# Kernel tuning notes

Measured on AMD Instinct MI355X. Metric: run time of the kernel, lower is better.

The kernel has to match this reference:

```python
import jax, jax.numpy as jnp
import numpy as np

B, L, D_IN, D_OUT = 4, 2048, 4096, 4096


def setup_inputs() -> dict:
    key = jax.random.key(0)
    k1, k2, k3, k4 = jax.random.split(key, 4)
    x = jax.random.normal(k1, (B, L, D_IN), dtype=jnp.float32)
    # base weight stored transposed as [in, out], like self.base = base.T
    base = jax.random.normal(k2, (D_IN, D_OUT), dtype=jnp.float32) * 0.02
    # binary delta sign mask in {0, 1}, stored transposed [in, out]
    mask = jax.random.randint(k3, (D_IN, D_OUT), 0, 2).astype(jnp.int32)
    # coeff = mean(|finetune - base|); a small positive scalar
    coeff = jax.random.uniform(k4, (1,), dtype=jnp.float32) * 0.01
    return {"x": x, "base": base, "coeff": coeff, "mask": mask}


def reference(x, base, coeff, mask):
    # Original: x @ base.T_stored + coeff * (x @ repeated_mask)
    # (t_coeff * x) @ mask == t_coeff * (x @ mask); we avoid materializing the
    # per-batch repeated mask since broadcasting the [in, out] mask is equivalent.
    m = mask.astype(x.dtype)            # {0,1} dequantized mask, [in, out]
    c = coeff[0].astype(x.dtype)
    return jnp.einsum('bld,de->ble', x, base) + c * jnp.einsum('bld,de->ble', x, m)
```

## Files before the change

kernel.cpp:

```cpp
#include <hip/hip_runtime.h>
#include <hip/hip_bf16.h>
#include <stdint.h>

#define DIN 4096
#define DOUT 4096
#define BK 64
#define NT (DIN / BK)

typedef __attribute__((ext_vector_type(8))) short short8;
typedef __attribute__((ext_vector_type(8))) unsigned short ushort8;
typedef __attribute__((ext_vector_type(4))) float f32x4;

__device__ inline unsigned short f2bf(float f) {
    union { float f; unsigned u; } v; v.f = f;
    unsigned r = v.u + 0x7fffu + ((v.u >> 16) & 1u);
    return (unsigned short)(r >> 16);
}

__global__ void cvt_x_kernel(const float* __restrict__ x, ushort* __restrict__ xb, long n8) {
    long i = (long)blockIdx.x * blockDim.x + threadIdx.x;
    if (i >= n8) return;
    const float4* p = (const float4*)(x + i * 8);
    float4 v0 = p[0], v1 = p[1];
    ushort8 o;
    o[0] = f2bf(v0.x); o[1] = f2bf(v0.y); o[2] = f2bf(v0.z); o[3] = f2bf(v0.w);
    o[4] = f2bf(v1.x); o[5] = f2bf(v1.y); o[6] = f2bf(v1.z); o[7] = f2bf(v1.w);
    *(ushort8*)(xb + i * 8) = o;
}

__global__ void make_wt_kernel(const float* __restrict__ base, const int* __restrict__ mask,
                               const float* __restrict__ coeff, ushort* __restrict__ wt) {
    __shared__ float tile[64][65];
    const float c = coeff[0];
    const int t = threadIdx.x;
    const int bd = blockIdx.x >> 6;
    const int be = blockIdx.x & 63;
    const int d0 = bd * 64, e0 = be * 64;
#pragma unroll
    for (int i = 0; i < 4; ++i) {
        int idx = i * 256 + t;
        int r = idx >> 4;
        int c4 = (idx & 15) << 2;
        const float4 bv = *(const float4*)(base + (size_t)(d0 + r) * DOUT + e0 + c4);
        const int4  mv = *(const int4*)(mask + (size_t)(d0 + r) * DOUT + e0 + c4);
        tile[r][c4 + 0] = bv.x + c * (float)mv.x;
        tile[r][c4 + 1] = bv.y + c * (float)mv.y;
        tile[r][c4 + 2] = bv.z + c * (float)mv.z;
        tile[r][c4 + 3] = bv.w + c * (float)mv.w;
    }
    __syncthreads();
#pragma unroll
    for (int i = 0; i < 8; ++i) {
        int idx = i * 256 + t;
        int r = idx >> 5;
        int p = (idx & 31) << 1;
        ushort2 o;
        o.x = f2bf(tile[p][r]);
        o.y = f2bf(tile[p + 1][r]);
        *(ushort2*)(wt + (size_t)(e0 + r) * DIN + d0 + p) = o;
    }
}


#define MFMA(d, va, vb) d = __builtin_amdgcn_mfma_f32_16x16x32_bf16(va, vb, d, 0, 0, 0)

#define GLL(P, L) \
    __builtin_amdgcn_global_load_lds( \
        (const __attribute__((address_space(1))) void*)(P), \
        (__attribute__((address_space(3))) void*)(L), 16, 0, 0)

#define RDA(BUF,KK,OH,MM) (*(const short8*)&lA[BUF][KK][aoff + (OH)*2048 + (MM)*512])
#define RDB(BUF,KK,NN)    (*(const short8*)&lB[BUF][KK][boff + (NN)*512])

#define STAGE_A(BUF,KK,OFE) { GLL(gA0 + (OFE), &lA[BUF][KK][doff]); \
                              GLL(gA1 + (OFE), &lA[BUF][KK][doff + 4096]); }
#define STAGE_B(BUF,KK,OFE) { GLL(gB0 + (OFE), &lB[BUF][KK][doff]); \
                              GLL(gB1 + (OFE), &lB[BUF][KK][doff + 4096]); }

#define PHASE_CORE(AOFF) \
    __builtin_amdgcn_s_barrier(); \
    asm volatile("s_waitcnt lgkmcnt(0)" ::: "memory"); \
    __builtin_amdgcn_sched_barrier(0); \
    __builtin_amdgcn_s_setprio(1); \
    MFMA(acc[AOFF+0][0],a0,b0); MFMA(acc[AOFF+0][1],a0,b1); MFMA(acc[AOFF+0][2],a0,b2); MFMA(acc[AOFF+0][3],a0,b3); \
    MFMA(acc[AOFF+1][0],a1,b0); MFMA(acc[AOFF+1][1],a1,b1); MFMA(acc[AOFF+1][2],a1,b2); MFMA(acc[AOFF+1][3],a1,b3); \
    MFMA(acc[AOFF+2][0],a2,b0); MFMA(acc[AOFF+2][1],a2,b1); MFMA(acc[AOFF+2][2],a2,b2); MFMA(acc[AOFF+2][3],a2,b3); \
    MFMA(acc[AOFF+3][0],a3,b0); MFMA(acc[AOFF+3][1],a3,b1); MFMA(acc[AOFF+3][2],a3,b2); MFMA(acc[AOFF+3][3],a3,b3); \
    __builtin_amdgcn_s_setprio(0);

#define KTILE(BUF, G1, G2, NEXT, OFE1, OFE2) \
  { \
    short8 a0,a1,a2,a3,b0,b1,b2,b3; \
    a0=RDA(BUF,0,0,0); a1=RDA(BUF,0,0,1); a2=RDA(BUF,0,0,2); a3=RDA(BUF,0,0,3); \
    b0=RDB(BUF,0,0); b1=RDB(BUF,0,1); b2=RDB(BUF,0,2); b3=RDB(BUF,0,3); \
    if (G1) STAGE_A(1-(BUF), 1, OFE1) \
    PHASE_CORE(0) \
    __builtin_amdgcn_s_barrier(); \
    a0=RDA(BUF,0,1,0); a1=RDA(BUF,0,1,1); a2=RDA(BUF,0,1,2); a3=RDA(BUF,0,1,3); \
    if (G1) STAGE_B(1-(BUF), 1, OFE1) \
    PHASE_CORE(4) \
    __builtin_amdgcn_s_barrier(); \
    a0=RDA(BUF,1,0,0); a1=RDA(BUF,1,0,1); a2=RDA(BUF,1,0,2); a3=RDA(BUF,1,0,3); \
    b0=RDB(BUF,1,0); b1=RDB(BUF,1,1); b2=RDB(BUF,1,2); b3=RDB(BUF,1,3); \
    if (G2) STAGE_A(BUF, 0, OFE2) \
    PHASE_CORE(0) \
    __builtin_amdgcn_s_barrier(); \
    a0=RDA(BUF,1,1,0); a1=RDA(BUF,1,1,1); a2=RDA(BUF,1,1,2); a3=RDA(BUF,1,1,3); \
    if (G2) STAGE_B(BUF, 0, OFE2) \
    PHASE_CORE(4) \
    if (G2)        { asm volatile("s_waitcnt vmcnt(4)" ::: "memory"); } \
    else if (NEXT) { asm volatile("s_waitcnt vmcnt(0)" ::: "memory"); } \
    __builtin_amdgcn_s_barrier(); \
    __builtin_amdgcn_sched_barrier(0); \
  }

__global__ __launch_bounds__(512, 2) void gemm_kernel(const ushort* __restrict__ A,
                                                      const ushort* __restrict__ Bt,
                                                      float* __restrict__ C) {
    __shared__ __align__(16) ushort lA[2][2][256 * 32];
    __shared__ __align__(16) ushort lB[2][2][256 * 32];

    const int tid = threadIdx.x;
    const int lane = tid & 63;
    const int wave = tid >> 6;

    const int nbn = DOUT / 256;
    const int nwg = gridDim.x;
    int bid = blockIdx.x;
    int cpx = nwg >> 3;
    int s = (bid & 7) * cpx + (bid >> 3);
    const int m0 = (s / nbn) * 256;
    const int n0 = (s % nbn) * 256;

    const int wr = wave >> 2;
    const int wc = wave & 3;
    const int fr = lane & 15;
    const int fq = lane >> 4;

    const int st_r = tid >> 2;
    const int st_c = (tid & 3) << 4;

    const int sx = ((fr >> 1) & 3) << 3;
    const int aoff = (wr * 128 + fr) * 32 + ((fq << 3) ^ sx);
    const int boff = (wc * 64 + fr) * 32 + ((fq << 3) ^ sx);
    const int doff = tid * 8;
    const int sce = ((tid & 3) << 3) ^ (((st_r >> 1) & 3) << 3);
    const ushort* gA0 = A  + (size_t)(m0 + st_r) * DIN + sce;
    const ushort* gA1 = gA0 + (size_t)128 * DIN;
    const ushort* gB0 = Bt + (size_t)(n0 + st_r) * DIN + sce;
    const ushort* gB1 = gB0 + (size_t)128 * DIN;

    f32x4 acc[8][4] = {};

    STAGE_A(0, 0, 0)   STAGE_B(0, 0, 0)
    STAGE_A(0, 1, 32)  STAGE_B(0, 1, 32)
    STAGE_A(1, 0, 64)  STAGE_B(1, 0, 64)
    asm volatile("s_waitcnt vmcnt(4)" ::: "memory");
    __builtin_amdgcn_s_barrier();
    __builtin_amdgcn_sched_barrier(0);

    for (int u = 0; u < NT; u += 2) {
        KTILE(0, 1, (u + 2 < NT), 1, 96, 128)
        KTILE(1, (u + 2 < NT), (u + 3 < NT), (u + 2 < NT), 160, 192)
        gA0 += 128; gA1 += 128; gB0 += 128; gB1 += 128;
    }

#pragma unroll
    for (int a = 0; a < 8; ++a) {
        int grow = m0 + wr * 128 + (a >> 2) * 64 + (a & 3) * 16 + fq * 4;
#pragma unroll
        for (int n = 0; n < 4; ++n) {
            int gcol = n0 + wc * 64 + n * 16 + fr;
#pragma unroll
            for (int j = 0; j < 4; ++j)
                C[(size_t)(grow + j) * DOUT + gcol] = acc[a][n][j];
        }
    }
}

extern "C" void kernel_launch(void* const* d_in, const int* in_sizes, int n_in,
                              void* d_out, int out_size, void* d_ws, size_t ws_size,
                              hipStream_t stream) {
    const float* x = (const float*)d_in[0];
    const float* base = (const float*)d_in[1];
    const float* coeff = (const float*)d_in[2];
    const int* mask = (const int*)d_in[3];
    float* out = (float*)d_out;

    const int M = in_sizes[0] / DIN;
    ushort* xb = (ushort*)d_ws;
    ushort* wt = xb + (size_t)M * DIN;

    long n8 = (long)M * DIN / 8;
    cvt_x_kernel<<<(int)((n8 + 255) / 256), 256, 0, stream>>>(x, xb, n8);
    make_wt_kernel<<<(DIN / 64) * (DOUT / 64), 256, 0, stream>>>(base, mask, coeff, wt);

    const int nwg = (M / 256) * (DOUT / 256);
    gemm_kernel<<<nwg, 512, 0, stream>>>(xb, wt, out);
}
```

Before: 323.8 us.

## Software-pipeline LDS fragment reads one phase ahead of MFMA groups

```diff
diff --git a/kernel.cpp b/kernel.cpp
--- a/kernel.cpp
+++ b/kernel.cpp
@@ -64,6 +64,12 @@
 
 #define MFMA(d, va, vb) d = __builtin_amdgcn_mfma_f32_16x16x32_bf16(va, vb, d, 0, 0, 0)
 
+#define MFMA16(AOFF, x0,x1,x2,x3, y0,y1,y2,y3) \
+    MFMA(acc[AOFF+0][0],x0,y0); MFMA(acc[AOFF+0][1],x0,y1); MFMA(acc[AOFF+0][2],x0,y2); MFMA(acc[AOFF+0][3],x0,y3); \
+    MFMA(acc[AOFF+1][0],x1,y0); MFMA(acc[AOFF+1][1],x1,y1); MFMA(acc[AOFF+1][2],x1,y2); MFMA(acc[AOFF+1][3],x1,y3); \
+    MFMA(acc[AOFF+2][0],x2,y0); MFMA(acc[AOFF+2][1],x2,y1); MFMA(acc[AOFF+2][2],x2,y2); MFMA(acc[AOFF+2][3],x2,y3); \
+    MFMA(acc[AOFF+3][0],x3,y0); MFMA(acc[AOFF+3][1],x3,y1); MFMA(acc[AOFF+3][2],x3,y2); MFMA(acc[AOFF+3][3],x3,y3);
+
 #define GLL(P, L) \
     __builtin_amdgcn_global_load_lds( \
         (const __attribute__((address_space(1))) void*)(P), \
@@ -77,41 +83,55 @@
 #define STAGE_B(BUF,KK,OFE) { GLL(gB0 + (OFE), &lB[BUF][KK][doff]); \
                               GLL(gB1 + (OFE), &lB[BUF][KK][doff + 4096]); }
 
-#define PHASE_CORE(AOFF) \
-    __builtin_amdgcn_s_barrier(); \
-    asm volatile("s_waitcnt lgkmcnt(0)" ::: "memory"); \
-    __builtin_amdgcn_sched_barrier(0); \
-    __builtin_amdgcn_s_setprio(1); \
-    MFMA(acc[AOFF+0][0],a0,b0); MFMA(acc[AOFF+0][1],a0,b1); MFMA(acc[AOFF+0][2],a0,b2); MFMA(acc[AOFF+0][3],a0,b3); \
-    MFMA(acc[AOFF+1][0],a1,b0); MFMA(acc[AOFF+1][1],a1,b1); MFMA(acc[AOFF+1][2],a1,b2); MFMA(acc[AOFF+1][3],a1,b3); \
-    MFMA(acc[AOFF+2][0],a2,b0); MFMA(acc[AOFF+2][1],a2,b1); MFMA(acc[AOFF+2][2],a2,b2); MFMA(acc[AOFF+2][3],a2,b3); \
-    MFMA(acc[AOFF+3][0],a3,b0); MFMA(acc[AOFF+3][1],a3,b1); MFMA(acc[AOFF+3][2],a3,b2); MFMA(acc[AOFF+3][3],a3,b3); \
-    __builtin_amdgcn_s_setprio(0);
+#define WAITL(N)  asm volatile("s_waitcnt lgkmcnt(" #N ")" ::: "memory")
+#define WAITV(N)  asm volatile("s_waitcnt vmcnt(" #N ")" ::: "memory")
+#define SCHEDB    __builtin_amdgcn_sched_barrier(0)
+#define SBAR      __builtin_amdgcn_s_barrier()
 
 #define KTILE(BUF, G1, G2, NEXT, OFE1, OFE2) \
   { \
-    short8 a0,a1,a2,a3,b0,b1,b2,b3; \
-    a0=RDA(BUF,0,0,0); a1=RDA(BUF,0,0,1); a2=RDA(BUF,0,0,2); a3=RDA(BUF,0,0,3); \
-    b0=RDB(BUF,0,0); b1=RDB(BUF,0,1); b2=RDB(BUF,0,2); b3=RDB(BUF,0,3); \
+     \
+    aQ0=RDA(BUF,0,1,0); aQ1=RDA(BUF,0,1,1); aQ2=RDA(BUF,0,1,2); aQ3=RDA(BUF,0,1,3); \
     if (G1) STAGE_A(1-(BUF), 1, OFE1) \
-    PHASE_CORE(0) \
-    __builtin_amdgcn_s_barrier(); \
-    a0=RDA(BUF,0,1,0); a1=RDA(BUF,0,1,1); a2=RDA(BUF,0,1,2); a3=RDA(BUF,0,1,3); \
+    SCHEDB; SBAR; \
+    WAITL(4); SCHEDB; \
+    __builtin_amdgcn_s_setprio(1); \
+    MFMA16(0, aP0,aP1,aP2,aP3, bP0,bP1,bP2,bP3) \
+    __builtin_amdgcn_s_setprio(0); \
+    SCHEDB; SBAR; \
+     \
+    WAITV(6); \
+    aP0=RDA(BUF,1,0,0); aP1=RDA(BUF,1,0,1); aP2=RDA(BUF,1,0,2); aP3=RDA(BUF,1,0,3); \
+    bQ0=RDB(BUF,1,0); bQ1=RDB(BUF,1,1); bQ2=RDB(BUF,1,2); bQ3=RDB(BUF,1,3); \
     if (G1) STAGE_B(1-(BUF), 1, OFE1) \
-    PHASE_CORE(4) \
-    __builtin_amdgcn_s_barrier(); \
-    a0=RDA(BUF,1,0,0); a1=RDA(BUF,1,0,1); a2=RDA(BUF,1,0,2); a3=RDA(BUF,1,0,3); \
-    b0=RDB(BUF,1,0); b1=RDB(BUF,1,1); b2=RDB(BUF,1,2); b3=RDB(BUF,1,3); \
+    SCHEDB; SBAR; \
+    WAITL(8); SCHEDB; \
+    __builtin_amdgcn_s_setprio(1); \
+    MFMA16(4, aQ0,aQ1,aQ2,aQ3, bP0,bP1,bP2,bP3) \
+    __builtin_amdgcn_s_setprio(0); \
+    SCHEDB; SBAR; \
+     \
+    aQ0=RDA(BUF,1,1,0); aQ1=RDA(BUF,1,1,1); aQ2=RDA(BUF,1,1,2); aQ3=RDA(BUF,1,1,3); \
     if (G2) STAGE_A(BUF, 0, OFE2) \
-    PHASE_CORE(0) \
-    __builtin_amdgcn_s_barrier(); \
-    a0=RDA(BUF,1,1,0); a1=RDA(BUF,1,1,1); a2=RDA(BUF,1,1,2); a3=RDA(BUF,1,1,3); \
+    SCHEDB; SBAR; \
+    WAITL(4); SCHEDB; \
+    __builtin_amdgcn_s_setprio(1); \
+    MFMA16(0, aP0,aP1,aP2,aP3, bQ0,bQ1,bQ2,bQ3) \
+    __builtin_amdgcn_s_setprio(0); \
+    SCHEDB; SBAR; \
+     \
+    WAITV(6); \
+    aP0=RDA(1-(BUF),0,0,0); aP1=RDA(1-(BUF),0,0,1); aP2=RDA(1-(BUF),0,0,2); aP3=RDA(1-(BUF),0,0,3); \
+    bP0=RDB(1-(BUF),0,0); bP1=RDB(1-(BUF),0,1); bP2=RDB(1-(BUF),0,2); bP3=RDB(1-(BUF),0,3); \
     if (G2) STAGE_B(BUF, 0, OFE2) \
-    PHASE_CORE(4) \
-    if (G2)        { asm volatile("s_waitcnt vmcnt(4)" ::: "memory"); } \
-    else if (NEXT) { asm volatile("s_waitcnt vmcnt(0)" ::: "memory"); } \
-    __builtin_amdgcn_s_barrier(); \
-    __builtin_amdgcn_sched_barrier(0); \
+    SCHEDB; SBAR; \
+    WAITL(8); SCHEDB; \
+    __builtin_amdgcn_s_setprio(1); \
+    MFMA16(4, aQ0,aQ1,aQ2,aQ3, bQ0,bQ1,bQ2,bQ3) \
+    __builtin_amdgcn_s_setprio(0); \
+    if (G2)        { WAITV(4); } \
+    else if (NEXT) { WAITV(0); } \
+    SCHEDB; SBAR; SCHEDB; \
   }
 
 __global__ __launch_bounds__(512, 2) void gemm_kernel(const ushort* __restrict__ A,
@@ -138,7 +158,6 @@
     const int fq = lane >> 4;
 
     const int st_r = tid >> 2;
-    const int st_c = (tid & 3) << 4;
 
     const int sx = ((fr >> 1) & 3) << 3;
     const int aoff = (wr * 128 + fr) * 32 + ((fq << 3) ^ sx);
@@ -151,13 +170,17 @@
     const ushort* gB1 = gB0 + (size_t)128 * DIN;
 
     f32x4 acc[8][4] = {};
+    short8 aP0, aP1, aP2, aP3, aQ0, aQ1, aQ2, aQ3;
+    short8 bP0, bP1, bP2, bP3, bQ0, bQ1, bQ2, bQ3;
 
     STAGE_A(0, 0, 0)   STAGE_B(0, 0, 0)
     STAGE_A(0, 1, 32)  STAGE_B(0, 1, 32)
     STAGE_A(1, 0, 64)  STAGE_B(1, 0, 64)
-    asm volatile("s_waitcnt vmcnt(4)" ::: "memory");
-    __builtin_amdgcn_s_barrier();
-    __builtin_amdgcn_sched_barrier(0);
+    WAITV(8);
+    SBAR;
+    aP0=RDA(0,0,0,0); aP1=RDA(0,0,0,1); aP2=RDA(0,0,0,2); aP3=RDA(0,0,0,3);
+    bP0=RDB(0,0,0);   bP1=RDB(0,0,1);   bP2=RDB(0,0,2);   bP3=RDB(0,0,3);
+    SCHEDB;
 
     for (int u = 0; u < NT; u += 2) {
         KTILE(0, 1, (u + 2 < NT), 1, 96, 128)
```

Measured after the change: 543.5 us. 1.68x slower.
